# Kernel optimization log

Hardware: AMD Instinct MI355X
Metric: run time of the kernel (lower is better)

The kernel has to match this reference:

```python
import jax, jax.numpy as jnp
import numpy as np

B, S, V, D = 64, 256, 50000, 300
NW, CL, CV, CD = 8192, 16, 500, 30
H, T, CH = 128, 17, 30


def setup_inputs() -> dict:
    key = jax.random.key(0)
    ks = jax.random.split(key, 32)
    f32 = jnp.float32
    def rn(k, shape, scale=0.1):
        return jax.random.normal(k, shape, dtype=f32) * scale
    inp = {}
    inp["char_emb"] = rn(ks[0], (CV, CD)).at[0].set(0.0)  # padding_idx=0
    inp["conv_w"] = rn(ks[1], (CH, CD, 3))  # OIH
    inp["conv_b"] = rn(ks[2], (CH,))
    inp["word_emb"] = rn(ks[3], (V, D))
    in0, in1 = D + CH, 2 * H
    inp["w_ih_l0"] = rn(ks[4], (2, 3 * H, in0))  # [dir, 3H, in]
    inp["w_hh_l0"] = rn(ks[5], (2, 3 * H, H))
    inp["b_ih_l0"] = rn(ks[6], (2, 3 * H))
    inp["b_hh_l0"] = rn(ks[7], (2, 3 * H))
    inp["w_ih_l1"] = rn(ks[8], (2, 3 * H, in1))
    inp["w_hh_l1"] = rn(ks[9], (2, 3 * H, H))
    inp["b_ih_l1"] = rn(ks[10], (2, 3 * H))
    inp["b_hh_l1"] = rn(ks[11], (2, 3 * H))
    inp["mlp_w1"] = rn(ks[12], (2 * H, H))
    inp["mlp_b1"] = rn(ks[13], (H,))
    inp["mlp_w2"] = rn(ks[14], (H, T))
    inp["mlp_b2"] = rn(ks[15], (T,))
    inp["crf_start"] = rn(ks[16], (T,))
    inp["crf_end"] = rn(ks[17], (T,))
    inp["crf_trans"] = rn(ks[18], (T, T))
    inp["batched_char_words"] = jax.random.randint(ks[19], (NW, CL), 0, CV)
    inp["batched_char_words_len"] = jax.random.randint(ks[20], (NW,), 1, CL + 1)
    inp["batched_char_word_index"] = jax.random.randint(ks[21], (B, S), 0, NW + 1)
    inp["batched_tokens"] = jax.random.randint(ks[22], (B, S), 0, V)
    inp["batched_tokens_len"] = jax.random.randint(ks[23], (B,), S // 2, S + 1)
    inp["target"] = jax.random.randint(ks[24], (B, S), 0, T)
    return inp


def _gru_dir(x, mask, w_ih, w_hh, b_ih, b_hh, reverse):
    # x: [B,S,I], mask: [B,S] bool. Masked (padded) steps carry hidden state
    # through unchanged, matching pack_padded_sequence semantics.
    xg = jnp.einsum('bsi,gi->sbg', x, w_ih) + b_ih  # [S,B,3H]
    m = mask.T  # [S,B]
    h0 = jnp.zeros((x.shape[0], w_hh.shape[1]), x.dtype)

    def step(h, inp):
        xt, mt = inp
        hg = h @ w_hh.T + b_hh
        xr, xz, xn = jnp.split(xt, 3, axis=-1)
        hr, hz, hn = jnp.split(hg, 3, axis=-1)
        r = jax.nn.sigmoid(xr + hr)
        z = jax.nn.sigmoid(xz + hz)
        n = jnp.tanh(xn + r * hn)
        hnew = (1.0 - z) * n + z * h
        h = jnp.where(mt[:, None], hnew, h)
        return h, h

    _, hs = jax.lax.scan(step, h0, (xg, m), reverse=reverse)
    return hs.transpose(1, 0, 2)  # [B,S,H]


def _bigru_layer(x, mask, w_ih, w_hh, b_ih, b_hh):
    fwd = _gru_dir(x, mask, w_ih[0], w_hh[0], b_ih[0], b_hh[0], False)
    bwd = _gru_dir(x, mask, w_ih[1], w_hh[1], b_ih[1], b_hh[1], True)
    return jnp.concatenate([fwd, bwd], axis=-1)


def _forward(char_emb, conv_w, conv_b, word_emb,
             w_ih_l0, w_hh_l0, b_ih_l0, b_hh_l0,
             w_ih_l1, w_hh_l1, b_ih_l1, b_hh_l1,
             mlp_w1, mlp_b1, mlp_w2, mlp_b2,
             crf_start, crf_end, crf_trans,
             batched_char_words, batched_char_word_index,
             batched_tokens, batched_tokens_len, target):
    # --- char CNN token encoder: conv1d(k=3, SAME) + relu + max-over-time ---
    ct = char_emb[batched_char_words]  # [NW,CL,CD]
    c = jax.lax.conv_general_dilated(ct.transpose(0, 2, 1), conv_w, (1,), 'SAME',
                                     dimension_numbers=('NCH', 'OIH', 'NCH'))
    c = jax.nn.relu(c + conv_b[None, :, None])
    tok_enc = jnp.max(c, axis=-1)  # [NW,CH]
    tok_enc = jnp.concatenate([jnp.zeros((1, tok_enc.shape[1]), tok_enc.dtype), tok_enc], axis=0)
    tok_idx = tok_enc[batched_char_word_index]  # [B,S,CH] (index 0 -> zeros)

    texts = jnp.concatenate([word_emb[batched_tokens], tok_idx], axis=-1)  # [B,S,D+CH]
    seq = batched_tokens.shape[1]
    mask = jnp.arange(seq)[None, :] < batched_tokens_len[:, None]  # [B,S]

    # --- 2-layer BiGRU ---
    h = _bigru_layer(texts, mask, w_ih_l0, w_hh_l0, b_ih_l0, b_hh_l0)
    h = _bigru_layer(h, mask, w_ih_l1, w_hh_l1, b_ih_l1, b_hh_l1)

    # --- MLP head -> emissions [B,S,17] ---
    h = jax.nn.relu(h @ mlp_w1 + mlp_b1)
    emissions = h @ mlp_w2 + mlp_b2

    # --- CRF negative log-likelihood, reduction='token_mean' ---
    maskf = mask.astype(emissions.dtype)
    emit_sc = jnp.take_along_axis(emissions, target[..., None], axis=-1)[..., 0]  # [B,S]
    trans_sc = crf_trans[target[:, :-1], target[:, 1:]]  # [B,S-1]
    score = crf_start[target[:, 0]] + emit_sc[:, 0]
    score = score + jnp.sum((trans_sc + emit_sc[:, 1:]) * maskf[:, 1:], axis=1)
    last_tags = jnp.take_along_axis(target, (batched_tokens_len - 1)[:, None], axis=1)[:, 0]
    score = score + crf_end[last_tags]

    alpha0 = crf_start[None, :] + emissions[:, 0]  # [B,T]
    em_rest = emissions[:, 1:].transpose(1, 0, 2)  # [S-1,B,T]
    m_rest = mask[:, 1:].T  # [S-1,B]

    def crf_step(alpha, inp):
        emit, mt = inp
        new = jax.nn.logsumexp(alpha[:, :, None] + crf_trans[None], axis=1) + emit
        return jnp.where(mt[:, None], new, alpha), None

    alpha, _ = jax.lax.scan(crf_step, alpha0, (em_rest, m_rest))
    log_z = jax.nn.logsumexp(alpha + crf_end[None, :], axis=1)
    llh = score - log_z
    return -(jnp.sum(llh) / jnp.sum(maskf))


def reference(char_emb, conv_w, conv_b, word_emb,
              w_ih_l0, w_hh_l0, b_ih_l0, b_hh_l0,
              w_ih_l1, w_hh_l1, b_ih_l1, b_hh_l1,
              mlp_w1, mlp_b1, mlp_w2, mlp_b2,
              crf_start, crf_end, crf_trans,
              batched_char_words, batched_char_words_len,
              batched_char_word_index, batched_tokens, batched_tokens_len, target):
    return _forward(char_emb, conv_w, conv_b, word_emb,
                    w_ih_l0, w_hh_l0, b_ih_l0, b_hh_l0,
                    w_ih_l1, w_hh_l1, b_ih_l1, b_hh_l1,
                    mlp_w1, mlp_b1, mlp_w2, mlp_b2,
                    crf_start, crf_end, crf_trans,
                    batched_char_words, batched_char_word_index,
                    batched_tokens, batched_tokens_len, target)
```

## Files before the change

### kernel.cpp

```cpp
#include <hip/hip_runtime.h>
#include <cstddef>

#define BATCH 64
#define SEQ   256
#define VOCAB 50000
#define DIM   300
#define NW    8192
#define CLEN  16
#define CDIM  30
#define CHC   30
#define HID   128
#define NT    17
#define IN0   (DIM + CHC)
#define IN1   (2 * HID)
#define NPOS  (BATCH * SEQ)

constexpr size_t SZ_XG    = 2ull * BATCH * SEQ * 384;
constexpr size_t SZ_TEXTS = (size_t)NPOS * IN0;
constexpr size_t SZ_H1    = (size_t)NPOS * 256;
constexpr size_t SZ_TOK   = 245792;
constexpr size_t SZ_EMIS  = (size_t)NPOS * NT;
constexpr size_t OFF_XG    = 0;
constexpr size_t OFF_TEXTS = OFF_XG + SZ_XG;
constexpr size_t OFF_H1    = OFF_TEXTS + SZ_TEXTS;
constexpr size_t OFF_TOK   = OFF_H1 + SZ_H1;
constexpr size_t OFF_EMIS  = OFF_TOK + SZ_TOK;
constexpr size_t OFF_LLH   = OFF_EMIS + SZ_EMIS;

__device__ __forceinline__ float sigm(float x) {
    return 1.f / (1.f + __expf(-x));
}
__device__ __forceinline__ float tanh_fast(float x) {
    x = fminf(fmaxf(x, -15.f), 15.f);
    float e = __expf(-2.f * x);
    return (1.f - e) / (1.f + e);
}

__global__ __launch_bounds__(256) void char_conv_k(
    const float* __restrict__ char_emb,
    const float* __restrict__ conv_w,
    const float* __restrict__ conv_b,
    const int*   __restrict__ words,
    float* __restrict__ tok_enc)
{
    __shared__ __align__(16) float cs[8][CLEN][CDIM];
    __shared__ float wsm[CHC * CDIM * 3];
    __shared__ float bs[CHC];
    int n0 = blockIdx.x * 8;
    int tid = threadIdx.x;
    for (int e = tid; e < CHC * CDIM * 3; e += 256) wsm[e] = conv_w[e];
    if (tid < CHC) bs[tid] = conv_b[tid];
    for (int e = tid; e < 8 * CLEN * CDIM; e += 256) {
        int wi = e / (CLEN * CDIM);
        int rem = e - wi * (CLEN * CDIM);
        int l = rem / CDIM;
        int i = rem - l * CDIM;
        int ci = words[(n0 + wi) * CLEN + l];
        cs[wi][l][i] = char_emb[ci * CDIM + i];
    }
    __syncthreads();
    int wi = tid >> 5;
    int o = tid & 31;
    if (o < CHC) {
        float best = -1e30f;
        for (int l = 0; l < CLEN; l++) {
            float s = 0.f;
            #pragma unroll
            for (int k = 0; k < 3; k++) {
                int ll = l + k - 1;
                if (ll >= 0 && ll < CLEN) {
                    #pragma unroll
                    for (int i = 0; i < CDIM; i++)
                        s += cs[wi][ll][i] * wsm[(o * CDIM + i) * 3 + k];
                }
            }
            best = fmaxf(best, s);
        }
        tok_enc[(size_t)(n0 + wi + 1) * CDIM + o] = fmaxf(best + bs[o], 0.f);
    }
}

__global__ __launch_bounds__(128) void build_texts_k(
    const float* __restrict__ word_emb,
    const float* __restrict__ tok_enc,
    const int*   __restrict__ tokens,
    const int*   __restrict__ widx,
    float* __restrict__ texts)
{
    int p = blockIdx.x;
    int tok = tokens[p];
    int ci = widx[p];
    float* o = texts + (size_t)p * IN0;
    const float* wr = word_emb + (size_t)tok * DIM;
    const float* tr = tok_enc + (size_t)ci * CDIM;
    for (int c = threadIdx.x; c < IN0; c += 128)
        o[c] = (c < DIM) ? wr[c] : tr[c - DIM];
}

#define GBM 128
#define GBN 128
#define GBK 16
__global__ __launch_bounds__(256) void gemm_xg_k(
    const float* __restrict__ A,
    const float* __restrict__ W,
    const float* __restrict__ bias,
    float* __restrict__ out,
    int K)
{
    __shared__ __align__(16) float As[GBK][GBM];
    __shared__ __align__(16) float Ws[GBK][GBN];
    int tid = threadIdx.x;
    int m0 = blockIdx.x * GBM;
    int n0 = blockIdx.y * GBN;
    int lrow = tid >> 1;
    int lk = (tid & 1) * 8;
    int ty = tid >> 4;
    int tx = tid & 15;

    float acc[8][8];
    #pragma unroll
    for (int i = 0; i < 8; i++)
        #pragma unroll
        for (int j = 0; j < 8; j++) acc[i][j] = 0.f;

    for (int k0 = 0; k0 < K; k0 += GBK) {
        #pragma unroll
        for (int j = 0; j < 8; j++) {
            int k = k0 + lk + j;
            float va = (k < K) ? A[(size_t)(m0 + lrow) * K + k] : 0.f;
            float vw = (k < K) ? W[(size_t)(n0 + lrow) * K + k] : 0.f;
            As[lk + j][lrow] = va;
            Ws[lk + j][lrow] = vw;
        }
        __syncthreads();
        #pragma unroll
        for (int k = 0; k < GBK; k++) {
            float4 a0 = *(const float4*)&As[k][ty * 8];
            float4 a1 = *(const float4*)&As[k][ty * 8 + 4];
            float4 b0 = *(const float4*)&Ws[k][tx * 8];
            float4 b1 = *(const float4*)&Ws[k][tx * 8 + 4];
            float av[8] = {a0.x, a0.y, a0.z, a0.w, a1.x, a1.y, a1.z, a1.w};
            float bv[8] = {b0.x, b0.y, b0.z, b0.w, b1.x, b1.y, b1.z, b1.w};
            #pragma unroll
            for (int i = 0; i < 8; i++)
                #pragma unroll
                for (int j = 0; j < 8; j++)
                    acc[i][j] += av[i] * bv[j];
        }
        __syncthreads();
    }
    int nb = n0 + tx * 8;
    int d = nb / 384;
    int g0 = nb - d * 384;
    float bvv[8];
    #pragma unroll
    for (int j = 0; j < 8; j++) bvv[j] = bias[nb + j];
    int mbase = m0 + ty * 8;
    #pragma unroll
    for (int i = 0; i < 8; i++) {
        int m = mbase + i;
        int b = m >> 8;
        int t = m & 255;
        float* op = out + (((size_t)(d * BATCH + b) * SEQ + t) * 384 + g0);
        #pragma unroll
        for (int j = 0; j < 8; j++) op[j] = acc[i][j] + bvv[j];
    }
}

__global__ __launch_bounds__(384, 2) void gru_rec_k(
    const float* __restrict__ xg,
    const float* __restrict__ w_hh,
    const float* __restrict__ b_hh,
    const int*   __restrict__ lens,
    float* __restrict__ out)
{
    int d = blockIdx.x & 1;
    int b = blockIdx.x >> 1;
    int g = threadIdx.x;
    __shared__ __align__(16) float h[HID];
    __shared__ float srz[256];

    float4 w[32];
    const float4* wr = (const float4*)(w_hh + ((size_t)d * 384 + g) * HID);
    #pragma unroll
    for (int i = 0; i < 32; i++) w[i] = wr[i];
    float bh = b_hh[d * 384 + g];
    int len = lens[b];

    if (g < HID) h[g] = 0.f;
    __syncthreads();

    const float* xgb = xg + ((size_t)(d * BATCH + b)) * SEQ * 384;
    float* outb = out + (size_t)b * SEQ * 256 + d * HID;

    for (int s = 0; s < SEQ; s++) {
        int t = d ? (SEQ - 1 - s) : s;
        float xv = xgb[(size_t)t * 384 + g];
        const float4* h4 = (const float4*)h;
        float sx = 0.f, sy = 0.f, sz = 0.f, sw = 0.f;
        #pragma unroll
        for (int i = 0; i < 32; i++) {
            float4 hv = h4[i];
            sx += w[i].x * hv.x;
            sy += w[i].y * hv.y;
            sz += w[i].z * hv.z;
            sw += w[i].w * hv.w;
        }
        float acc = bh + ((sx + sy) + (sz + sw));
        if (g < 256) srz[g] = sigm(xv + acc);
        __syncthreads();
        if (g >= 256) {
            int j = g - 256;
            float r = srz[j];
            float z = srz[HID + j];
            float n = tanh_fast(xv + r * acc);
            float hold = h[j];
            float hnew = (1.f - z) * n + z * hold;
            float hv = (t < len) ? hnew : hold;
            h[j] = hv;
            outb[(size_t)t * 256 + j] = hv;
        }
        __syncthreads();
    }
}

__global__ __launch_bounds__(128) void mlp_emis_k(
    const float* __restrict__ h1,
    const float* __restrict__ w1,
    const float* __restrict__ b1,
    const float* __restrict__ w2,
    const float* __restrict__ b2,
    float* __restrict__ emis)
{
    __shared__ __align__(16) float hrow[8 * 256];
    __shared__ float hid[8][HID];
    int p0 = blockIdx.x * 8;
    int tid = threadIdx.x;
    for (int e = tid; e < 8 * 256; e += 128)
        hrow[e] = h1[(size_t)p0 * 256 + e];
    __syncthreads();
    float acc[8];
    float bb = b1[tid];
    #pragma unroll
    for (int i = 0; i < 8; i++) acc[i] = bb;
    for (int k = 0; k < 256; k++) {
        float wv = w1[k * HID + tid];
        #pragma unroll
        for (int i = 0; i < 8; i++) acc[i] += hrow[i * 256 + k] * wv;
    }
    #pragma unroll
    for (int i = 0; i < 8; i++) hid[i][tid] = fmaxf(acc[i], 0.f);
    __syncthreads();
    for (int idx = tid; idx < 8 * NT; idx += 128) {
        int pos = idx / NT;
        int tg = idx - pos * NT;
        float a = b2[tg];
        for (int k = 0; k < HID; k++) a += hid[pos][k] * w2[k * NT + tg];
        emis[(size_t)(p0 + pos) * NT + tg] = a;
    }
}

__global__ __launch_bounds__(64) void crf_k(
    const float* __restrict__ emis,
    const float* __restrict__ start,
    const float* __restrict__ endv,
    const float* __restrict__ trans,
    const int*   __restrict__ target,
    const int*   __restrict__ lens,
    float* __restrict__ llh)
{
    int b = blockIdx.x;
    int tid = threadIdx.x;
    __shared__ float tr[NT * NT];
    __shared__ float aSh[NT];
    __shared__ float scoreSh;
    for (int e = tid; e < NT * NT; e += 64) tr[e] = trans[e];
    __syncthreads();
    int len = lens[b];
    const int* tgt = target + b * SEQ;
    const float* eb = emis + (size_t)b * SEQ * NT;

    float part = 0.f;
    for (int t = 1 + tid; t < SEQ; t += 64) {
        if (t < len) {
            int tp = tgt[t - 1], tc = tgt[t];
            part += tr[tp * NT + tc] + eb[(size_t)t * NT + tc];
        }
    }
    #pragma unroll
    for (int off = 32; off > 0; off >>= 1)
        part += __shfl_down(part, off, 64);
    if (tid == 0) {
        int t0 = tgt[0];
        scoreSh = part + start[t0] + eb[t0] + endv[tgt[len - 1]];
    }

    float a = (tid < NT) ? (start[tid] + eb[tid]) : 0.f;
    for (int t = 1; t < SEQ; t++) {
        if (tid < NT) aSh[tid] = a;
        __syncthreads();
        if (t < len && tid < NT) {
            float m = -1e30f;
            #pragma unroll
            for (int i = 0; i < NT; i++)
                m = fmaxf(m, aSh[i] + tr[i * NT + tid]);
            float ssum = 0.f;
            #pragma unroll
            for (int i = 0; i < NT; i++)
                ssum += __expf(aSh[i] + tr[i * NT + tid] - m);
            a = m + __logf(ssum) + eb[(size_t)t * NT + tid];
        }
        __syncthreads();
    }
    float v = (tid < NT) ? (a + endv[tid]) : -1e30f;
    float m = v;
    #pragma unroll
    for (int off = 32; off > 0; off >>= 1)
        m = fmaxf(m, __shfl_down(m, off, 64));
    m = __shfl(m, 0, 64);
    float e = (tid < NT) ? __expf(v - m) : 0.f;
    #pragma unroll
    for (int off = 32; off > 0; off >>= 1)
        e += __shfl_down(e, off, 64);
    if (tid == 0) {
        float logz = m + __logf(e);
        llh[b] = scoreSh - logz;
    }
}

__global__ __launch_bounds__(64) void finalize_k(
    const float* __restrict__ llh,
    const int*   __restrict__ lens,
    float* __restrict__ out)
{
    int tid = threadIdx.x;
    float s = llh[tid];
    float lf = (float)lens[tid];
    #pragma unroll
    for (int off = 32; off > 0; off >>= 1) {
        s += __shfl_down(s, off, 64);
        lf += __shfl_down(lf, off, 64);
    }
    if (tid == 0) out[0] = -(s / lf);
}

extern "C" void kernel_launch(void* const* d_in, const int* in_sizes, int n_in,
                              void* d_out, int out_size, void* d_ws, size_t ws_size,
                              hipStream_t stream) {
    const float* char_emb = (const float*)d_in[0];
    const float* conv_w   = (const float*)d_in[1];
    const float* conv_b   = (const float*)d_in[2];
    const float* word_emb = (const float*)d_in[3];
    const float* w_ih_l0  = (const float*)d_in[4];
    const float* w_hh_l0  = (const float*)d_in[5];
    const float* b_ih_l0  = (const float*)d_in[6];
    const float* b_hh_l0  = (const float*)d_in[7];
    const float* w_ih_l1  = (const float*)d_in[8];
    const float* w_hh_l1  = (const float*)d_in[9];
    const float* b_ih_l1  = (const float*)d_in[10];
    const float* b_hh_l1  = (const float*)d_in[11];
    const float* mlp_w1   = (const float*)d_in[12];
    const float* mlp_b1   = (const float*)d_in[13];
    const float* mlp_w2   = (const float*)d_in[14];
    const float* mlp_b2   = (const float*)d_in[15];
    const float* crf_start= (const float*)d_in[16];
    const float* crf_end  = (const float*)d_in[17];
    const float* crf_trans= (const float*)d_in[18];
    const int* bcw   = (const int*)d_in[19];
    const int* bcwi  = (const int*)d_in[21];
    const int* btok  = (const int*)d_in[22];
    const int* blen  = (const int*)d_in[23];
    const int* target= (const int*)d_in[24];

    float* ws    = (float*)d_ws;
    float* xg    = ws + OFF_XG;
    float* texts = ws + OFF_TEXTS;
    float* h0    = texts;
    float* h1    = ws + OFF_H1;
    float* tok   = ws + OFF_TOK;
    float* emis  = ws + OFF_EMIS;
    float* llh   = ws + OFF_LLH;

    hipMemsetAsync(tok, 0, CDIM * sizeof(float), stream);
    char_conv_k<<<NW / 8, 256, 0, stream>>>(char_emb, conv_w, conv_b, bcw, tok);
    build_texts_k<<<NPOS, 128, 0, stream>>>(word_emb, tok, btok, bcwi, texts);
    gemm_xg_k<<<dim3(NPOS / GBM, 768 / GBN), 256, 0, stream>>>(texts, w_ih_l0, b_ih_l0, xg, IN0);
    gru_rec_k<<<2 * BATCH, 384, 0, stream>>>(xg, w_hh_l0, b_hh_l0, blen, h0);
    gemm_xg_k<<<dim3(NPOS / GBM, 768 / GBN), 256, 0, stream>>>(h0, w_ih_l1, b_ih_l1, xg, IN1);
    gru_rec_k<<<2 * BATCH, 384, 0, stream>>>(xg, w_hh_l1, b_hh_l1, blen, h1);
    mlp_emis_k<<<NPOS / 8, 128, 0, stream>>>(h1, mlp_w1, mlp_b1, mlp_w2, mlp_b2, emis);
    crf_k<<<BATCH, 64, 0, stream>>>(emis, crf_start, crf_end, crf_trans, target, blen, llh);
    finalize_k<<<1, 64, 0, stream>>>(llh, blen, (float*)d_out);
}
```

Before: 1.051 ms.

## Halve GRU block threads, prefetch gate inputs, and vectorize padded GEMM loads

The GRU recurrence kernel now runs 192 threads per block, each holding two rows of the hidden-hidden weight matrix in registers. Each shared-memory read of the hidden state therefore feeds two dot products. The next step's input-gate values are prefetched one iteration ahead to hide global-load latency on the serial chain. The layer-0 input and weight matrices are padded to K=336 so the GEMM tile loader can use float4 loads without bounds checks. This costs an extra padding kernel and more workspace, and the doubled register-resident weights risk spills or longer per-step arithmetic.

After: 1.199 ms. +14.1%, slower.

```diff
diff --git a/kernel.cpp b/kernel.cpp
--- a/kernel.cpp
+++ b/kernel.cpp
@@ -12,20 +12,23 @@
 #define HID   128
 #define NT    17
 #define IN0   (DIM + CHC)
+#define IN0P  336
 #define IN1   (2 * HID)
 #define NPOS  (BATCH * SEQ)
 
 constexpr size_t SZ_XG    = 2ull * BATCH * SEQ * 384;
-constexpr size_t SZ_TEXTS = (size_t)NPOS * IN0;
+constexpr size_t SZ_TEXTS = (size_t)NPOS * IN0P;
 constexpr size_t SZ_H1    = (size_t)NPOS * 256;
 constexpr size_t SZ_TOK   = 245792;
 constexpr size_t SZ_EMIS  = (size_t)NPOS * NT;
+constexpr size_t SZ_WPAD  = 768ull * IN0P;
 constexpr size_t OFF_XG    = 0;
 constexpr size_t OFF_TEXTS = OFF_XG + SZ_XG;
 constexpr size_t OFF_H1    = OFF_TEXTS + SZ_TEXTS;
 constexpr size_t OFF_TOK   = OFF_H1 + SZ_H1;
 constexpr size_t OFF_EMIS  = OFF_TOK + SZ_TOK;
-constexpr size_t OFF_LLH   = OFF_EMIS + SZ_EMIS;
+constexpr size_t OFF_WPAD  = OFF_EMIS + SZ_EMIS;
+constexpr size_t OFF_LLH   = OFF_WPAD + SZ_WPAD;
 
 __device__ __forceinline__ float sigm(float x) {
     return 1.f / (1.f + __expf(-x));
@@ -90,11 +93,19 @@
     int p = blockIdx.x;
     int tok = tokens[p];
     int ci = widx[p];
-    float* o = texts + (size_t)p * IN0;
+    float* o = texts + (size_t)p * IN0P;
     const float* wr = word_emb + (size_t)tok * DIM;
     const float* tr = tok_enc + (size_t)ci * CDIM;
-    for (int c = threadIdx.x; c < IN0; c += 128)
-        o[c] = (c < DIM) ? wr[c] : tr[c - DIM];
+    for (int c = threadIdx.x; c < IN0P; c += 128)
+        o[c] = (c < DIM) ? wr[c] : (c < IN0 ? tr[c - DIM] : 0.f);
+}
+
+__global__ __launch_bounds__(64) void pad_w_k(
+    const float* __restrict__ w, float* __restrict__ wp)
+{
+    int r = blockIdx.x;
+    for (int c = threadIdx.x; c < IN0P; c += 64)
+        wp[(size_t)r * IN0P + c] = (c < IN0) ? w[(size_t)r * IN0 + c] : 0.f;
 }
 
 #define GBM 128
@@ -124,14 +135,18 @@
         for (int j = 0; j < 8; j++) acc[i][j] = 0.f;
 
     for (int k0 = 0; k0 < K; k0 += GBK) {
-        #pragma unroll
-        for (int j = 0; j < 8; j++) {
-            int k = k0 + lk + j;
-            float va = (k < K) ? A[(size_t)(m0 + lrow) * K + k] : 0.f;
-            float vw = (k < K) ? W[(size_t)(n0 + lrow) * K + k] : 0.f;
-            As[lk + j][lrow] = va;
-            Ws[lk + j][lrow] = vw;
-        }
+        const float4* ap = (const float4*)(A + (size_t)(m0 + lrow) * K + k0 + lk);
+        const float4* wp = (const float4*)(W + (size_t)(n0 + lrow) * K + k0 + lk);
+        float4 va0 = ap[0], va1 = ap[1];
+        float4 vw0 = wp[0], vw1 = wp[1];
+        As[lk + 0][lrow] = va0.x; As[lk + 1][lrow] = va0.y;
+        As[lk + 2][lrow] = va0.z; As[lk + 3][lrow] = va0.w;
+        As[lk + 4][lrow] = va1.x; As[lk + 5][lrow] = va1.y;
+        As[lk + 6][lrow] = va1.z; As[lk + 7][lrow] = va1.w;
+        Ws[lk + 0][lrow] = vw0.x; Ws[lk + 1][lrow] = vw0.y;
+        Ws[lk + 2][lrow] = vw0.z; Ws[lk + 3][lrow] = vw0.w;
+        Ws[lk + 4][lrow] = vw1.x; Ws[lk + 5][lrow] = vw1.y;
+        Ws[lk + 6][lrow] = vw1.z; Ws[lk + 7][lrow] = vw1.w;
         __syncthreads();
         #pragma unroll
         for (int k = 0; k < GBK; k++) {
@@ -167,7 +182,7 @@
     }
 }
 
-__global__ __launch_bounds__(384, 2) void gru_rec_k(
+__global__ __launch_bounds__(192, 1) void gru_rec_k(
     const float* __restrict__ xg,
     const float* __restrict__ w_hh,
     const float* __restrict__ b_hh,
@@ -176,44 +191,63 @@
 {
     int d = blockIdx.x & 1;
     int b = blockIdx.x >> 1;
-    int g = threadIdx.x;
+    int i = threadIdx.x;
+    int row0 = i;
+    int row1 = i + 192;
     __shared__ __align__(16) float h[HID];
     __shared__ float srz[256];
 
-    float4 w[32];
-    const float4* wr = (const float4*)(w_hh + ((size_t)d * 384 + g) * HID);
-    #pragma unroll
-    for (int i = 0; i < 32; i++) w[i] = wr[i];
-    float bh = b_hh[d * 384 + g];
+    float4 w0[32], w1[32];
+    {
+        const float4* wr0 = (const float4*)(w_hh + ((size_t)d * 384 + row0) * HID);
+        const float4* wr1 = (const float4*)(w_hh + ((size_t)d * 384 + row1) * HID);
+        #pragma unroll
+        for (int q = 0; q < 32; q++) { w0[q] = wr0[q]; w1[q] = wr1[q]; }
+    }
+    float bh0 = b_hh[d * 384 + row0];
+    float bh1 = b_hh[d * 384 + row1];
     int len = lens[b];
 
-    if (g < HID) h[g] = 0.f;
+    if (i < HID) h[i] = 0.f;
     __syncthreads();
 
     const float* xgb = xg + ((size_t)(d * BATCH + b)) * SEQ * 384;
     float* outb = out + (size_t)b * SEQ * 256 + d * HID;
 
+    int t0 = d ? (SEQ - 1) : 0;
+    float pxv0 = xgb[(size_t)t0 * 384 + row0];
+    float pxv1 = xgb[(size_t)t0 * 384 + row1];
+
     for (int s = 0; s < SEQ; s++) {
         int t = d ? (SEQ - 1 - s) : s;
-        float xv = xgb[(size_t)t * 384 + g];
+        float xv0 = pxv0, xv1 = pxv1;
+        int sn = (s + 1 < SEQ) ? (s + 1) : s;
+        int tn = d ? (SEQ - 1 - sn) : sn;
+        pxv0 = xgb[(size_t)tn * 384 + row0];
+        pxv1 = xgb[(size_t)tn * 384 + row1];
+
         const float4* h4 = (const float4*)h;
-        float sx = 0.f, sy = 0.f, sz = 0.f, sw = 0.f;
-        #pragma unroll
-        for (int i = 0; i < 32; i++) {
-            float4 hv = h4[i];
-            sx += w[i].x * hv.x;
-            sy += w[i].y * hv.y;
-            sz += w[i].z * hv.z;
-            sw += w[i].w * hv.w;
-        }
-        float acc = bh + ((sx + sy) + (sz + sw));
-        if (g < 256) srz[g] = sigm(xv + acc);
-        __syncthreads();
-        if (g >= 256) {
-            int j = g - 256;
+        float a0x = 0.f, a0y = 0.f, a0z = 0.f, a0w = 0.f;
+        float a1x = 0.f, a1y = 0.f, a1z = 0.f, a1w = 0.f;
+        #pragma unroll
+        for (int q = 0; q < 32; q++) {
+            float4 hv = h4[q];
+            a0x += w0[q].x * hv.x; a0y += w0[q].y * hv.y;
+            a0z += w0[q].z * hv.z; a0w += w0[q].w * hv.w;
+            a1x += w1[q].x * hv.x; a1y += w1[q].y * hv.y;
+            a1z += w1[q].z * hv.z; a1w += w1[q].w * hv.w;
+        }
+        float acc0 = bh0 + ((a0x + a0y) + (a0z + a0w));
+        float acc1 = bh1 + ((a1x + a1y) + (a1z + a1w));
+
+        srz[row0] = sigm(xv0 + acc0);
+        if (row1 < 256) srz[row1] = sigm(xv1 + acc1);
+        __syncthreads();
+        if (i >= 64) {
+            int j = i - 64;
             float r = srz[j];
             float z = srz[HID + j];
-            float n = tanh_fast(xv + r * acc);
+            float n = tanh_fast(xv1 + r * acc1);
             float hold = h[j];
             float hnew = (1.f - z) * n + z * hold;
             float hv = (t < len) ? hnew : hold;
@@ -379,15 +413,17 @@
     float* h1    = ws + OFF_H1;
     float* tok   = ws + OFF_TOK;
     float* emis  = ws + OFF_EMIS;
+    float* wpad  = ws + OFF_WPAD;
     float* llh   = ws + OFF_LLH;
 
     hipMemsetAsync(tok, 0, CDIM * sizeof(float), stream);
+    pad_w_k<<<768, 64, 0, stream>>>(w_ih_l0, wpad);
     char_conv_k<<<NW / 8, 256, 0, stream>>>(char_emb, conv_w, conv_b, bcw, tok);
     build_texts_k<<<NPOS, 128, 0, stream>>>(word_emb, tok, btok, bcwi, texts);
-    gemm_xg_k<<<dim3(NPOS / GBM, 768 / GBN), 256, 0, stream>>>(texts, w_ih_l0, b_ih_l0, xg, IN0);
-    gru_rec_k<<<2 * BATCH, 384, 0, stream>>>(xg, w_hh_l0, b_hh_l0, blen, h0);
+    gemm_xg_k<<<dim3(NPOS / GBM, 768 / GBN), 256, 0, stream>>>(texts, wpad, b_ih_l0, xg, IN0P);
+    gru_rec_k<<<2 * BATCH, 192, 0, stream>>>(xg, w_hh_l0, b_hh_l0, blen, h0);
     gemm_xg_k<<<dim3(NPOS / GBM, 768 / GBN), 256, 0, stream>>>(h0, w_ih_l1, b_ih_l1, xg, IN1);
-    gru_rec_k<<<2 * BATCH, 384, 0, stream>>>(xg, w_hh_l1, b_hh_l1, blen, h1);
+    gru_rec_k<<<2 * BATCH, 192, 0, stream>>>(xg, w_hh_l1, b_hh_l1, blen, h1);
     mlp_emis_k<<<NPOS / 8, 128, 0, stream>>>(h1, mlp_w1, mlp_b1, mlp_w2, mlp_b2, emis);
     crf_k<<<BATCH, 64, 0, stream>>>(emis, crf_start, crf_end, crf_trans, target, blen, llh);
     finalize_k<<<1, 64, 0, stream>>>(llh, blen, (float*)d_out);
```
